# Kernel tuning notes

Measured on AMD Instinct MI355X. Metric: run time of the kernel, lower is better.

Reference implementation:

```python
import jax, jax.numpy as jnp
import numpy as np

N_VOXELS = 262144  # active output voxels (stride=1 -> same coord set as input)


def setup_inputs() -> dict:
    key = jax.random.key(0)
    k1, k2, k3, k4 = jax.random.split(key, 4)
    N, C_IN, C_OUT, K, M = N_VOXELS, 64, 64, 27, 65536
    x = jax.random.normal(k1, (N, C_IN), dtype=jnp.float32)
    W = jax.random.normal(k2, (K, C_IN, C_OUT), dtype=jnp.float32) * (1.0 / np.sqrt(C_IN * K))
    in_map = jax.random.randint(k3, (K, M), 0, N, dtype=jnp.int32)
    out_map = jax.random.randint(k4, (K, M), 0, N, dtype=jnp.int32)
    return {"x": x, "W": W, "in_map": in_map, "out_map": out_map}


def reference(x, W, in_map, out_map):
    # Sparse (Minkowski-style) convolution: gather -> per-offset GEMM -> scatter-add.
    # x: [N, Cin], W: [K, Cin, Cout], in_map/out_map: [K, M] indices into voxel list.
    N = x.shape[0]
    C_out = W.shape[-1]
    gathered = x[in_map]                              # [K, M, Cin]  (irregular gather)
    msg = jnp.einsum('kmc,kcd->kmd', gathered, W)     # [K, M, Cout] per-offset GEMM
    out = jnp.zeros((N, C_out), dtype=x.dtype)
    out = out.at[out_map.reshape(-1)].add(msg.reshape(-1, C_out))  # scatter-add
    return out
```

## Files before the change

kernel.cpp:

```cpp
#include <hip/hip_runtime.h>


typedef __attribute__((ext_vector_type(8))) short bf16x8;
typedef __attribute__((ext_vector_type(8))) unsigned short u16x8;
typedef __attribute__((ext_vector_type(4))) unsigned short u16x4;
typedef __attribute__((ext_vector_type(4))) float f32x4;
typedef __attribute__((ext_vector_type(2))) float f32x2;

constexpr int KOFF = 27;
constexpr int M = 65536;
constexpr int CIN = 64;
constexpr int COUT = 64;
constexpr int NVOX = 262144;
constexpr int NMSG = KOFF * M;
constexpr int TM_BLOCK = 512;
constexpr int TILES_PER_K = M / TM_BLOCK;
constexpr int SUBTILES = TM_BLOCK / (4 * 16);
constexpr int XCVT_BLOCKS = NVOX * CIN / 8 / 256;

static __device__ __forceinline__ short f2bf(float f) {
  unsigned u = __builtin_bit_cast(unsigned, f);
  unsigned r = (u + 0x7FFFu + ((u >> 16) & 1u)) >> 16;
  return (short)r;
}
static __device__ __forceinline__ float bf2f(unsigned short h) {
  return __builtin_bit_cast(float, (unsigned)h << 16);
}


__global__ __launch_bounds__(256) void xw_kernel(
    const float* __restrict__ x, const float* __restrict__ W,
    unsigned short* __restrict__ xb, unsigned short* __restrict__ Wf,
    int xcvtBlocks) {
  const int b = blockIdx.x;
  if (b < xcvtBlocks) {
    int i = b * 256 + threadIdx.x;
    const float4* p = (const float4*)x + (size_t)i * 2;
    float4 a = p[0], q = p[1];
    u16x8 h;
    h[0] = (unsigned short)f2bf(a.x); h[1] = (unsigned short)f2bf(a.y);
    h[2] = (unsigned short)f2bf(a.z); h[3] = (unsigned short)f2bf(a.w);
    h[4] = (unsigned short)f2bf(q.x); h[5] = (unsigned short)f2bf(q.y);
    h[6] = (unsigned short)f2bf(q.z); h[7] = (unsigned short)f2bf(q.w);
    *(u16x8*)(xb + (size_t)i * 8) = h;
  } else {
    int k = b - xcvtBlocks;
    const float* Wk = W + (size_t)k * (CIN * COUT);
    unsigned short* dst = Wf + (size_t)k * 4096;
#pragma unroll
    for (int i = 0; i < 16; ++i) {
      int e = threadIdx.x * 16 + i;
      int j = e & 7, l = (e >> 3) & 63, tu = e >> 9;
      int t = tu >> 1, u = tu & 1;
      dst[e] = (unsigned short)f2bf(Wk[(u * 32 + (l >> 4) * 8 + j) * COUT + t * 16 + (l & 15)]);
    }
  }
}


__global__ __launch_bounds__(256) void rank_kernel(const int* __restrict__ out_map,
                                                   int* __restrict__ cnt,
                                                   int* __restrict__ rank) {
  int i = (blockIdx.x * 256 + threadIdx.x) * 4;
  int4 om = *(const int4*)(out_map + i);
  int4 rk;
  rk.x = atomicAdd(&cnt[om.x], 1);
  rk.y = atomicAdd(&cnt[om.y], 1);
  rk.z = atomicAdd(&cnt[om.z], 1);
  rk.w = atomicAdd(&cnt[om.w], 1);
  *(int4*)(rank + i) = rk;
}


__global__ __launch_bounds__(256) void scan1_kernel(const int* __restrict__ cnt,
                                                    int* __restrict__ starts,
                                                    int* __restrict__ blockSums) {
  __shared__ int s[256];
  int t = threadIdx.x, i = blockIdx.x * 256 + t;
  int c = cnt[i];
  s[t] = c; __syncthreads();
  for (int off = 1; off < 256; off <<= 1) {
    int add = (t >= off) ? s[t - off] : 0;
    __syncthreads(); s[t] += add; __syncthreads();
  }
  starts[i] = s[t] - c;
  if (t == 255) blockSums[blockIdx.x] = s[t];
}

__global__ __launch_bounds__(256) void scan2_kernel(int* __restrict__ bs) {
  __shared__ int s[256];
  int t = threadIdx.x;
  int v0 = bs[t*4], v1 = bs[t*4+1], v2 = bs[t*4+2], v3 = bs[t*4+3];
  int sum = v0 + v1 + v2 + v3;
  s[t] = sum; __syncthreads();
  for (int off = 1; off < 256; off <<= 1) {
    int add = (t >= off) ? s[t - off] : 0;
    __syncthreads(); s[t] += add; __syncthreads();
  }
  int run = s[t] - sum;
  bs[t*4] = run; run += v0;
  bs[t*4+1] = run; run += v1;
  bs[t*4+2] = run; run += v2;
  bs[t*4+3] = run;
}

__global__ __launch_bounds__(256) void scan3_kernel(int* __restrict__ starts,
                                                    const int* __restrict__ blockBase) {
  int i = blockIdx.x * 256 + threadIdx.x;
  starts[i] += blockBase[blockIdx.x];
  if (i == 0) starts[NVOX] = NMSG;
}


__global__ __launch_bounds__(256) void listscat_kernel(
    const int* __restrict__ out_map, const int* __restrict__ rank,
    const int* __restrict__ starts, int* __restrict__ list) {
  int i = (blockIdx.x * 256 + threadIdx.x) * 4;
  int4 om = *(const int4*)(out_map + i);
  int4 rk = *(const int4*)(rank + i);
  list[starts[om.x] + rk.x] = i;
  list[starts[om.y] + rk.y] = i + 1;
  list[starts[om.z] + rk.z] = i + 2;
  list[starts[om.w] + rk.w] = i + 3;
}


template <bool BF16IN>
__global__ __launch_bounds__(256) void gemm_msg_kernel(
    const void* __restrict__ xin, const unsigned short* __restrict__ Wf,
    const int* __restrict__ in_map, unsigned short* __restrict__ msg) {
  const int k = blockIdx.x / TILES_PER_K;
  const int mblock = (blockIdx.x % TILES_PER_K) * TM_BLOCK;
  const int wave = threadIdx.x >> 6;
  const int l = threadIdx.x & 63;
  const int lg = l >> 4;
  const int lr = l & 15;

  bf16x8 bfrag[4][2];
  const bf16x8* wf = (const bf16x8*)(Wf + (size_t)k * 4096);
#pragma unroll
  for (int t = 0; t < 4; ++t)
#pragma unroll
    for (int u = 0; u < 2; ++u)
      bfrag[t][u] = wf[(t * 2 + u) * 64 + l];

  const int mwave = mblock + wave * (TM_BLOCK / 4);
  const int rb = k * M + mwave;

  auto loadA = [&](int s, bf16x8& A0, bf16x8& A1) {
    int id = in_map[rb + s * 16 + lr];
    if (BF16IN) {
      const unsigned short* xr = (const unsigned short*)xin + (size_t)id * CIN + lg * 8;
      A0 = *(const bf16x8*)(xr);
      A1 = *(const bf16x8*)(xr + 32);
    } else {
      const float* xr = (const float*)xin + (size_t)id * CIN + lg * 8;
      float4 x0 = *(const float4*)(xr);
      float4 x1 = *(const float4*)(xr + 4);
      float4 x2 = *(const float4*)(xr + 32);
      float4 x3 = *(const float4*)(xr + 36);
      A0[0]=f2bf(x0.x); A0[1]=f2bf(x0.y); A0[2]=f2bf(x0.z); A0[3]=f2bf(x0.w);
      A0[4]=f2bf(x1.x); A0[5]=f2bf(x1.y); A0[6]=f2bf(x1.z); A0[7]=f2bf(x1.w);
      A1[0]=f2bf(x2.x); A1[1]=f2bf(x2.y); A1[2]=f2bf(x2.z); A1[3]=f2bf(x2.w);
      A1[4]=f2bf(x3.x); A1[5]=f2bf(x3.y); A1[6]=f2bf(x3.z); A1[7]=f2bf(x3.w);
    }
  };

  bf16x8 c0, c1, n0, n1;
  loadA(0, c0, c1);
  loadA(1, n0, n1);

#pragma unroll 1
  for (int s = 0; s < SUBTILES; ++s) {
    bf16x8 p0, p1;
    const bool have = (s + 2 < SUBTILES);
    if (have) loadA(s + 2, p0, p1);

    f32x4 acc[4] = {{0.f,0.f,0.f,0.f},{0.f,0.f,0.f,0.f},{0.f,0.f,0.f,0.f},{0.f,0.f,0.f,0.f}};
#pragma unroll
    for (int t = 0; t < 4; ++t) {
      acc[t] = __builtin_amdgcn_mfma_f32_16x16x32_bf16(c0, bfrag[t][0], acc[t], 0, 0, 0);
      acc[t] = __builtin_amdgcn_mfma_f32_16x16x32_bf16(c1, bfrag[t][1], acc[t], 0, 0, 0);
    }

    const size_t rowb = (size_t)(rb + s * 16 + lg * 4);
#pragma unroll
    for (int r = 0; r < 4; ++r) {
      u16x4 h;
      h[0] = (unsigned short)f2bf(acc[0][r]);
      h[1] = (unsigned short)f2bf(acc[1][r]);
      h[2] = (unsigned short)f2bf(acc[2][r]);
      h[3] = (unsigned short)f2bf(acc[3][r]);
      __builtin_nontemporal_store(h, (u16x4*)(msg + (rowb + r) * 64 + lr * 4));
    }

    c0 = n0; c1 = n1;
    if (have) { n0 = p0; n1 = p1; }
  }
}


__global__ __launch_bounds__(256) void gather_out_kernel(
    const unsigned short* __restrict__ msg, const int* __restrict__ starts,
    const int* __restrict__ list, float* __restrict__ out) {
  const int wid = (blockIdx.x * 256 + threadIdx.x) >> 6;
  const int p = threadIdx.x & 63;
  const int r = p >> 3;
  const int c = p & 7;
  const int o = wid * 8 + r;

  const int base = starts[o];
  const int n = starts[o + 1] - base;

  int li[8];
#pragma unroll
  for (int i = 0; i < 8; ++i) {
    int idx = base + ((i < n) ? i : 0);
    li[i] = list[idx < NMSG ? idx : 0];
  }
  u16x8 v[8];
#pragma unroll
  for (int i = 0; i < 8; ++i)
    v[i] = __builtin_nontemporal_load((const u16x8*)(msg + (size_t)li[i] * 64 + c * 8));

  float acc[8] = {};
#pragma unroll
  for (int i = 0; i < 8; ++i) {
    float m = (i < n) ? 1.0f : 0.0f;
#pragma unroll
    for (int d = 0; d < 8; ++d)
      acc[d] = fmaf(m, bf2f((unsigned short)v[i][d]), acc[d]);
  }
  for (int i = 8; i < n; ++i) {
    int idx = list[base + i];
    u16x8 t = __builtin_nontemporal_load((const u16x8*)(msg + (size_t)idx * 64 + c * 8));
#pragma unroll
    for (int d = 0; d < 8; ++d) acc[d] += bf2f((unsigned short)t[d]);
  }

  float* orow = out + (size_t)o * 64 + 2 * c;
  f32x2 s0 = {acc[0], acc[4]};
  f32x2 s1 = {acc[1], acc[5]};
  f32x2 s2 = {acc[2], acc[6]};
  f32x2 s3 = {acc[3], acc[7]};
  __builtin_nontemporal_store(s0, (f32x2*)(orow));
  __builtin_nontemporal_store(s1, (f32x2*)(orow + 16));
  __builtin_nontemporal_store(s2, (f32x2*)(orow + 32));
  __builtin_nontemporal_store(s3, (f32x2*)(orow + 48));
}


__global__ __launch_bounds__(256) void spconv_atomic_kernel(
    const float* __restrict__ x, const float* __restrict__ W,
    const int* __restrict__ in_map, const int* __restrict__ out_map,
    float* __restrict__ out) {
  const int k = blockIdx.x / TILES_PER_K;
  const int mblock = (blockIdx.x % TILES_PER_K) * TM_BLOCK;
  const int wave = threadIdx.x >> 6;
  const int l = threadIdx.x & 63;
  const int lg = l >> 4;
  const int lr = l & 15;
  bf16x8 bfrag[4][2];
  const float* Wk = W + (size_t)k * (CIN * COUT);
#pragma unroll
  for (int t = 0; t < 4; ++t)
#pragma unroll
    for (int u = 0; u < 2; ++u)
#pragma unroll
      for (int j = 0; j < 8; ++j)
        bfrag[t][u][j] = f2bf(Wk[(u * 32 + lg * 8 + j) * COUT + t * 16 + lr]);
  const int mwave = mblock + wave * (TM_BLOCK / 4);
#pragma unroll 1
  for (int s = 0; s < SUBTILES; ++s) {
    const int mbase = mwave + s * 16;
    const int in_idx = in_map[k * M + mbase + lr];
    const float* xr = x + (size_t)in_idx * CIN + lg * 8;
    float4 x0 = *(const float4*)(xr);
    float4 x1 = *(const float4*)(xr + 4);
    float4 x2 = *(const float4*)(xr + 32);
    float4 x3 = *(const float4*)(xr + 36);
    bf16x8 a0, a1;
    a0[0]=f2bf(x0.x); a0[1]=f2bf(x0.y); a0[2]=f2bf(x0.z); a0[3]=f2bf(x0.w);
    a0[4]=f2bf(x1.x); a0[5]=f2bf(x1.y); a0[6]=f2bf(x1.z); a0[7]=f2bf(x1.w);
    a1[0]=f2bf(x2.x); a1[1]=f2bf(x2.y); a1[2]=f2bf(x2.z); a1[3]=f2bf(x2.w);
    a1[4]=f2bf(x3.x); a1[5]=f2bf(x3.y); a1[6]=f2bf(x3.z); a1[7]=f2bf(x3.w);
    f32x4 acc[4] = {{0.f,0.f,0.f,0.f},{0.f,0.f,0.f,0.f},{0.f,0.f,0.f,0.f},{0.f,0.f,0.f,0.f}};
#pragma unroll
    for (int t = 0; t < 4; ++t) {
      acc[t] = __builtin_amdgcn_mfma_f32_16x16x32_bf16(a0, bfrag[t][0], acc[t], 0, 0, 0);
      acc[t] = __builtin_amdgcn_mfma_f32_16x16x32_bf16(a1, bfrag[t][1], acc[t], 0, 0, 0);
    }
    const int obase = k * M + mbase + lg * 4;
    int oidx[4];
#pragma unroll
    for (int r = 0; r < 4; ++r) oidx[r] = out_map[obase + r];
#pragma unroll
    for (int t = 0; t < 4; ++t)
#pragma unroll
      for (int r = 0; r < 4; ++r)
        atomicAdd(out + (size_t)oidx[r] * COUT + t * 16 + lr, acc[t][r]);
  }
}

extern "C" void kernel_launch(void* const* d_in, const int* in_sizes, int n_in,
                              void* d_out, int out_size, void* d_ws, size_t ws_size,
                              hipStream_t stream) {
  const float* x = (const float*)d_in[0];
  const float* W = (const float*)d_in[1];
  const int* in_map = (const int*)d_in[2];
  const int* out_map = (const int*)d_in[3];
  float* out = (float*)d_out;
  char* ws = (char*)d_ws;

  const size_t msg_b    = (size_t)NMSG * 128;
  const size_t xb_b     = (size_t)NVOX * CIN * 2;
  const size_t list_b   = (size_t)NMSG * 4;
  const size_t wf_b     = (size_t)KOFF * 4096 * 2;
  const size_t starts_b = (size_t)(NVOX + 1) * 4;
  const size_t cnt_b    = (size_t)NVOX * 4;
  const size_t rank_b   = (size_t)NMSG * 4;
  auto pad = [](size_t b) { return (b + 255) & ~(size_t)255; };

  size_t need_p1 = pad(msg_b) + pad(list_b) + pad(wf_b) + pad(starts_b);
  size_t need_p0 = need_p1 + pad(xb_b);
  bool useXb = (ws_size >= need_p0);
  bool outScratchOk =
      ((size_t)out_size * 4 >= pad(cnt_b) + pad(1024 * 4) + pad(rank_b));

  if (ws_size < need_p1 || !outScratchOk) {
    hipMemsetAsync(d_out, 0, (size_t)out_size * sizeof(float), stream);
    spconv_atomic_kernel<<<dim3(KOFF * TILES_PER_K), dim3(256), 0, stream>>>(
        x, W, in_map, out_map, out);
    return;
  }

  size_t off = 0;
  unsigned short* msg = (unsigned short*)(ws + off); off += pad(msg_b);
  unsigned short* xb = nullptr;
  if (useXb) { xb = (unsigned short*)(ws + off); off += pad(xb_b); }
  int* list = (int*)(ws + off); off += pad(list_b);
  unsigned short* Wf = (unsigned short*)(ws + off); off += pad(wf_b);
  int* starts = (int*)(ws + off); off += pad(starts_b);

  char* outs = (char*)d_out;
  size_t ooff = 0;
  int* cnt  = (int*)(outs + ooff); ooff += pad(cnt_b);
  int* bsum = (int*)(outs + ooff); ooff += pad(1024 * 4);
  int* rank = (int*)(outs + ooff);

  hipMemsetAsync(cnt, 0, cnt_b, stream);

  int xcvtBlocks = useXb ? XCVT_BLOCKS : 0;
  xw_kernel<<<dim3(xcvtBlocks + KOFF), dim3(256), 0, stream>>>(x, W, xb, Wf, xcvtBlocks);

  rank_kernel<<<dim3(NMSG / 1024), dim3(256), 0, stream>>>(out_map, cnt, rank);

  scan1_kernel<<<dim3(NVOX / 256), dim3(256), 0, stream>>>(cnt, starts, bsum);
  scan2_kernel<<<dim3(1), dim3(256), 0, stream>>>(bsum);
  scan3_kernel<<<dim3(NVOX / 256), dim3(256), 0, stream>>>(starts, bsum);

  listscat_kernel<<<dim3(NMSG / 1024), dim3(256), 0, stream>>>(out_map, rank, starts, list);

  if (useXb)
    gemm_msg_kernel<true><<<dim3(KOFF * TILES_PER_K), dim3(256), 0, stream>>>(
        (const void*)xb, Wf, in_map, msg);
  else
    gemm_msg_kernel<false><<<dim3(KOFF * TILES_PER_K), dim3(256), 0, stream>>>(
        (const void*)x, Wf, in_map, msg);

  gather_out_kernel<<<dim3(NVOX / 32), dim3(256), 0, stream>>>(msg, starts, list, out);
}
```

Baseline: 259.9 us.

## Scatter GEMM messages into output-sorted order so the reduction reads contiguously

Instead of building a list of message indices grouped by output voxel, the code computes each message's destination slot, and the GEMM kernel writes each message row directly to that slot in output-sorted order. The reduction kernel then reads contiguous runs of message rows per output voxel, with no list indirection. In exchange, the GEMM kernel's stores become scattered 8-byte writes instead of sequential nontemporal stores. The fp32 fallback path inside the GEMM is also dropped, so the bf16 copy of x is now required.

```diff
diff --git a/kernel.cpp b/kernel.cpp
--- a/kernel.cpp
+++ b/kernel.cpp
@@ -112,23 +112,25 @@
 }
 
 
-__global__ __launch_bounds__(256) void listscat_kernel(
+__global__ __launch_bounds__(256) void permcalc_kernel(
     const int* __restrict__ out_map, const int* __restrict__ rank,
-    const int* __restrict__ starts, int* __restrict__ list) {
+    const int* __restrict__ starts, int* __restrict__ perm) {
   int i = (blockIdx.x * 256 + threadIdx.x) * 4;
   int4 om = *(const int4*)(out_map + i);
   int4 rk = *(const int4*)(rank + i);
-  list[starts[om.x] + rk.x] = i;
-  list[starts[om.y] + rk.y] = i + 1;
-  list[starts[om.z] + rk.z] = i + 2;
-  list[starts[om.w] + rk.w] = i + 3;
-}
-
-
-template <bool BF16IN>
+  int4 p;
+  p.x = starts[om.x] + rk.x;
+  p.y = starts[om.y] + rk.y;
+  p.z = starts[om.z] + rk.z;
+  p.w = starts[om.w] + rk.w;
+  *(int4*)(perm + i) = p;
+}
+
+
 __global__ __launch_bounds__(256) void gemm_msg_kernel(
-    const void* __restrict__ xin, const unsigned short* __restrict__ Wf,
-    const int* __restrict__ in_map, unsigned short* __restrict__ msg) {
+    const unsigned short* __restrict__ xb, const unsigned short* __restrict__ Wf,
+    const int* __restrict__ in_map, const int* __restrict__ perm,
+    unsigned short* __restrict__ msg) {
   const int k = blockIdx.x / TILES_PER_K;
   const int mblock = (blockIdx.x % TILES_PER_K) * TM_BLOCK;
   const int wave = threadIdx.x >> 6;
@@ -149,21 +151,9 @@
 
   auto loadA = [&](int s, bf16x8& A0, bf16x8& A1) {
     int id = in_map[rb + s * 16 + lr];
-    if (BF16IN) {
-      const unsigned short* xr = (const unsigned short*)xin + (size_t)id * CIN + lg * 8;
-      A0 = *(const bf16x8*)(xr);
-      A1 = *(const bf16x8*)(xr + 32);
-    } else {
-      const float* xr = (const float*)xin + (size_t)id * CIN + lg * 8;
-      float4 x0 = *(const float4*)(xr);
-      float4 x1 = *(const float4*)(xr + 4);
-      float4 x2 = *(const float4*)(xr + 32);
-      float4 x3 = *(const float4*)(xr + 36);
-      A0[0]=f2bf(x0.x); A0[1]=f2bf(x0.y); A0[2]=f2bf(x0.z); A0[3]=f2bf(x0.w);
-      A0[4]=f2bf(x1.x); A0[5]=f2bf(x1.y); A0[6]=f2bf(x1.z); A0[7]=f2bf(x1.w);
-      A1[0]=f2bf(x2.x); A1[1]=f2bf(x2.y); A1[2]=f2bf(x2.z); A1[3]=f2bf(x2.w);
-      A1[4]=f2bf(x3.x); A1[5]=f2bf(x3.y); A1[6]=f2bf(x3.z); A1[7]=f2bf(x3.w);
-    }
+    const unsigned short* xr = xb + (size_t)id * CIN + lg * 8;
+    A0 = *(const bf16x8*)(xr);
+    A1 = *(const bf16x8*)(xr + 32);
   };
 
   bf16x8 c0, c1, n0, n1;
@@ -183,15 +173,16 @@
       acc[t] = __builtin_amdgcn_mfma_f32_16x16x32_bf16(c1, bfrag[t][1], acc[t], 0, 0, 0);
     }
 
-    const size_t rowb = (size_t)(rb + s * 16 + lg * 4);
+    const int* pr = perm + rb + s * 16 + lg * 4;
 #pragma unroll
     for (int r = 0; r < 4; ++r) {
+      const int sl = pr[r];
       u16x4 h;
       h[0] = (unsigned short)f2bf(acc[0][r]);
       h[1] = (unsigned short)f2bf(acc[1][r]);
       h[2] = (unsigned short)f2bf(acc[2][r]);
       h[3] = (unsigned short)f2bf(acc[3][r]);
-      __builtin_nontemporal_store(h, (u16x4*)(msg + (rowb + r) * 64 + lr * 4));
+      *(u16x4*)(msg + (size_t)sl * 64 + lr * 4) = h;
     }
 
     c0 = n0; c1 = n1;
@@ -202,7 +193,7 @@
 
 __global__ __launch_bounds__(256) void gather_out_kernel(
     const unsigned short* __restrict__ msg, const int* __restrict__ starts,
-    const int* __restrict__ list, float* __restrict__ out) {
+    float* __restrict__ out) {
   const int wid = (blockIdx.x * 256 + threadIdx.x) >> 6;
   const int p = threadIdx.x & 63;
   const int r = p >> 3;
@@ -211,18 +202,14 @@
 
   const int base = starts[o];
   const int n = starts[o + 1] - base;
-
-  int li[8];
+  const unsigned short* src = msg + (size_t)base * 64 + c * 8;
+
+  u16x8 v[8];
 #pragma unroll
   for (int i = 0; i < 8; ++i) {
-    int idx = base + ((i < n) ? i : 0);
-    li[i] = list[idx < NMSG ? idx : 0];
-  }
-  u16x8 v[8];
-#pragma unroll
-  for (int i = 0; i < 8; ++i)
-    v[i] = __builtin_nontemporal_load((const u16x8*)(msg + (size_t)li[i] * 64 + c * 8));
-
+    int safe = (i < n) ? i : 0;
+    v[i] = *(const u16x8*)(src + (size_t)safe * 64);
+  }
   float acc[8] = {};
 #pragma unroll
   for (int i = 0; i < 8; ++i) {
@@ -232,8 +219,7 @@
       acc[d] = fmaf(m, bf2f((unsigned short)v[i][d]), acc[d]);
   }
   for (int i = 8; i < n; ++i) {
-    int idx = list[base + i];
-    u16x8 t = __builtin_nontemporal_load((const u16x8*)(msg + (size_t)idx * 64 + c * 8));
+    u16x8 t = *(const u16x8*)(src + (size_t)i * 64);
 #pragma unroll
     for (int d = 0; d < 8; ++d) acc[d] += bf2f((unsigned short)t[d]);
   }
@@ -314,20 +300,18 @@
 
   const size_t msg_b    = (size_t)NMSG * 128;
   const size_t xb_b     = (size_t)NVOX * CIN * 2;
-  const size_t list_b   = (size_t)NMSG * 4;
+  const size_t perm_b   = (size_t)NMSG * 4;
   const size_t wf_b     = (size_t)KOFF * 4096 * 2;
   const size_t starts_b = (size_t)(NVOX + 1) * 4;
   const size_t cnt_b    = (size_t)NVOX * 4;
   const size_t rank_b   = (size_t)NMSG * 4;
   auto pad = [](size_t b) { return (b + 255) & ~(size_t)255; };
 
-  size_t need_p1 = pad(msg_b) + pad(list_b) + pad(wf_b) + pad(starts_b);
-  size_t need_p0 = need_p1 + pad(xb_b);
-  bool useXb = (ws_size >= need_p0);
+  size_t need = pad(msg_b) + pad(xb_b) + pad(perm_b) + pad(wf_b) + pad(starts_b);
   bool outScratchOk =
       ((size_t)out_size * 4 >= pad(cnt_b) + pad(1024 * 4) + pad(rank_b));
 
-  if (ws_size < need_p1 || !outScratchOk) {
+  if (ws_size < need || !outScratchOk) {
     hipMemsetAsync(d_out, 0, (size_t)out_size * sizeof(float), stream);
     spconv_atomic_kernel<<<dim3(KOFF * TILES_PER_K), dim3(256), 0, stream>>>(
         x, W, in_map, out_map, out);
@@ -336,11 +320,10 @@
 
   size_t off = 0;
   unsigned short* msg = (unsigned short*)(ws + off); off += pad(msg_b);
-  unsigned short* xb = nullptr;
-  if (useXb) { xb = (unsigned short*)(ws + off); off += pad(xb_b); }
-  int* list = (int*)(ws + off); off += pad(list_b);
+  unsigned short* xb  = (unsigned short*)(ws + off); off += pad(xb_b);
+  int* perm = (int*)(ws + off); off += pad(perm_b);
   unsigned short* Wf = (unsigned short*)(ws + off); off += pad(wf_b);
-  int* starts = (int*)(ws + off); off += pad(starts_b);
+  int* starts = (int*)(ws + off);
 
   char* outs = (char*)d_out;
   size_t ooff = 0;
@@ -350,23 +333,17 @@
 
   hipMemsetAsync(cnt, 0, cnt_b, stream);
 
-  int xcvtBlocks = useXb ? XCVT_BLOCKS : 0;
-  xw_kernel<<<dim3(xcvtBlocks + KOFF), dim3(256), 0, stream>>>(x, W, xb, Wf, xcvtBlocks);
-
+  xw_kernel<<<dim3(XCVT_BLOCKS + KOFF), dim3(256), 0, stream>>>(x, W, xb, Wf, XCVT_BLOCKS);
   rank_kernel<<<dim3(NMSG / 1024), dim3(256), 0, stream>>>(out_map, cnt, rank);
 
   scan1_kernel<<<dim3(NVOX / 256), dim3(256), 0, stream>>>(cnt, starts, bsum);
   scan2_kernel<<<dim3(1), dim3(256), 0, stream>>>(bsum);
   scan3_kernel<<<dim3(NVOX / 256), dim3(256), 0, stream>>>(starts, bsum);
 
-  listscat_kernel<<<dim3(NMSG / 1024), dim3(256), 0, stream>>>(out_map, rank, starts, list);
-
-  if (useXb)
-    gemm_msg_kernel<true><<<dim3(KOFF * TILES_PER_K), dim3(256), 0, stream>>>(
-        (const void*)xb, Wf, in_map, msg);
-  else
-    gemm_msg_kernel<false><<<dim3(KOFF * TILES_PER_K), dim3(256), 0, stream>>>(
-        (const void*)x, Wf, in_map, msg);
-
-  gather_out_kernel<<<dim3(NVOX / 32), dim3(256), 0, stream>>>(msg, starts, list, out);
-}
+  permcalc_kernel<<<dim3(NMSG / 1024), dim3(256), 0, stream>>>(out_map, rank, starts, perm);
+
+  gemm_msg_kernel<<<dim3(KOFF * TILES_PER_K), dim3(256), 0, stream>>>(
+      xb, Wf, in_map, perm, msg);
+
+  gather_out_kernel<<<dim3(NVOX / 32), dim3(256), 0, stream>>>(msg, starts, out);
+}
```

After: 244.6 us. -5.9%, faster.
